# Performance work log

Hardware: AMD Instinct MI355X
Metric: run time of the kernel (lower is better)

## Reference

```python
import jax, jax.numpy as jnp
import numpy as np

VOCAB = 50257
EMBED = 1024


def setup_inputs() -> dict:
    key = jax.random.key(0)
    ks = jax.random.split(key, 8)
    s = 1.0 / np.sqrt(EMBED)  # PyTorch LSTM init scale (for realistic magnitudes)
    return {
        "input": jax.random.randint(ks[0], (1,), 0, VOCAB, dtype=jnp.int64),
        "hidden_state": jax.random.normal(ks[1], (1, 1, EMBED), dtype=jnp.float32),
        "cell_state": jax.random.normal(ks[2], (1, 1, EMBED), dtype=jnp.float32),
        "embed_table": jax.random.normal(ks[3], (VOCAB, EMBED), dtype=jnp.float32),
        "W_ih": jax.random.normal(ks[4], (4 * EMBED, EMBED), dtype=jnp.float32) * s,
        "W_hh": jax.random.normal(ks[5], (4 * EMBED, EMBED), dtype=jnp.float32) * s,
        "b_ih": jax.random.normal(ks[6], (4 * EMBED,), dtype=jnp.float32) * s,
        "b_hh": jax.random.normal(ks[7], (4 * EMBED,), dtype=jnp.float32) * s,
    }


def reference(input, hidden_state, cell_state, embed_table, W_ih, W_hh, b_ih, b_hh):
    # Embedding lookup: token id -> [EMBED]
    x = embed_table[input[0]]                      # [E]
    h = hidden_state[0, 0]                         # [E]
    c = cell_state[0, 0]                           # [E]
    # Single LSTM step, PyTorch gate order: i, f, g, o
    gates = W_ih @ x + b_ih + W_hh @ h + b_hh      # [4E]
    i, f, g, o = jnp.split(gates, 4)
    i = jax.nn.sigmoid(i)
    f = jax.nn.sigmoid(f)
    g = jnp.tanh(g)
    o = jax.nn.sigmoid(o)
    c_new = f * c + i * g
    h_new = o * jnp.tanh(c_new)
    return (h_new.reshape(1, 1, EMBED), c_new.reshape(1, 1, EMBED))
```

## Files before the change

### kernel.cpp

```cpp
#include <hip/hip_runtime.h>
#include <math.h>

#define EMBED 1024

__device__ __forceinline__ float dot4(float4 a, float4 b) {
    return a.x * b.x + a.y * b.y + a.z * b.z + a.w * b.w;
}

__global__ __launch_bounds__(256) void lstm_step_kernel(
    const unsigned int* __restrict__ tok,
    const float* __restrict__ h_in,
    const float* __restrict__ c_in,
    const float* __restrict__ embed,
    const float* __restrict__ W_ih,
    const float* __restrict__ W_hh,
    const float* __restrict__ b_ih,
    const float* __restrict__ b_hh,
    float* __restrict__ out)
{
    __shared__ float x_s[EMBED];
    __shared__ float h_s[EMBED];
    __shared__ float gate_s[4];

    const int tid  = threadIdx.x;
    const int j    = blockIdx.x;
    const int w    = tid >> 6;
    const int lane = tid & 63;
    const int row  = w * EMBED + j;

    const float4* wi = (const float4*)(W_ih + (size_t)row * EMBED);
    const float4* wh = (const float4*)(W_hh + (size_t)row * EMBED);
    float4 a0 = wi[lane];
    float4 a1 = wi[lane + 64];
    float4 a2 = wi[lane + 128];
    float4 a3 = wi[lane + 192];
    float4 b0 = wh[lane];
    float4 b1 = wh[lane + 64];
    float4 b2 = wh[lane + 128];
    float4 b3 = wh[lane + 192];

    const float bias  = b_ih[row] + b_hh[row];
    const float c_val = c_in[j];

    const unsigned int t = tok[0];
    const float* xrow = embed + (size_t)t * EMBED;
    ((float4*)x_s)[tid] = ((const float4*)xrow)[tid];
    ((float4*)h_s)[tid] = ((const float4*)h_in)[tid];
    __syncthreads();

    const float4* xs4 = (const float4*)x_s;
    const float4* hs4 = (const float4*)h_s;

    float acc;
    acc  = dot4(a0, xs4[lane]);
    acc += dot4(a1, xs4[lane + 64]);
    acc += dot4(a2, xs4[lane + 128]);
    acc += dot4(a3, xs4[lane + 192]);
    acc += dot4(b0, hs4[lane]);
    acc += dot4(b1, hs4[lane + 64]);
    acc += dot4(b2, hs4[lane + 128]);
    acc += dot4(b3, hs4[lane + 192]);

    #pragma unroll
    for (int off = 32; off > 0; off >>= 1)
        acc += __shfl_xor(acc, off);

    if (lane == 0)
        gate_s[w] = acc + bias;
    __syncthreads();

    if (tid == 0) {
        const float gi = gate_s[0];
        const float gf = gate_s[1];
        const float gg = gate_s[2];
        const float go = gate_s[3];
        const float i = 1.f / (1.f + __expf(-gi));
        const float f = 1.f / (1.f + __expf(-gf));
        const float e2g = __expf(2.f * gg);
        const float g = (e2g - 1.f) / (e2g + 1.f);
        const float o = 1.f / (1.f + __expf(-go));
        const float c_new = f * c_val + i * g;
        const float e2c = __expf(2.f * c_new);
        const float tc  = (e2c - 1.f) / (e2c + 1.f);
        const float h_new = o * tc;
        out[j]         = h_new;
        out[EMBED + j] = c_new;
    }
}

extern "C" void kernel_launch(void* const* d_in, const int* in_sizes, int n_in,
                              void* d_out, int out_size, void* d_ws, size_t ws_size,
                              hipStream_t stream) {
    const unsigned int* tok  = (const unsigned int*)d_in[0];
    const float* h_in  = (const float*)d_in[1];
    const float* c_in  = (const float*)d_in[2];
    const float* embed = (const float*)d_in[3];
    const float* W_ih  = (const float*)d_in[4];
    const float* W_hh  = (const float*)d_in[5];
    const float* b_ih  = (const float*)d_in[6];
    const float* b_hh  = (const float*)d_in[7];
    float* out = (float*)d_out;

    lstm_step_kernel<<<EMBED, 256, 0, stream>>>(
        tok, h_in, c_in, embed, W_ih, W_hh, b_ih, b_hh, out);
}
```

Before: 9.995 us.

## Split each gate row across two wavefronts and drop shared-memory vector staging

Each block now runs 512 threads (8 wavefronts), giving each of W_ih and W_hh its own wavefront per gate, so each thread loads half as many weight vectors. The x and h vectors are read straight from global memory into registers instead of being staged through LDS, which removes the first __syncthreads. The two partial sums are added in thread 0 before the activations are applied. This raises parallelism and memory-level concurrency on a bandwidth-bound GEMV, at the cost of redundant global reads of x/h that rely on the cache.

```diff
diff --git a/kernel.cpp b/kernel.cpp
--- a/kernel.cpp
+++ b/kernel.cpp
@@ -3,11 +3,13 @@
 
 #define EMBED 1024
 
-__device__ __forceinline__ float dot4(float4 a, float4 b) {
-    return a.x * b.x + a.y * b.y + a.z * b.z + a.w * b.w;
+typedef float f32x4 __attribute__((ext_vector_type(4)));
+
+__device__ __forceinline__ float dot4(f32x4 a, f32x4 b) {
+    return a[0] * b[0] + a[1] * b[1] + a[2] * b[2] + a[3] * b[3];
 }
 
-__global__ __launch_bounds__(256) void lstm_step_kernel(
+__global__ __launch_bounds__(512) void lstm_step_kernel(
     const unsigned int* __restrict__ tok,
     const float* __restrict__ h_in,
     const float* __restrict__ c_in,
@@ -18,62 +20,54 @@
     const float* __restrict__ b_hh,
     float* __restrict__ out)
 {
-    __shared__ float x_s[EMBED];
-    __shared__ float h_s[EMBED];
-    __shared__ float gate_s[4];
+    __shared__ float part[8];
 
     const int tid  = threadIdx.x;
     const int j    = blockIdx.x;
     const int w    = tid >> 6;
     const int lane = tid & 63;
-    const int row  = w * EMBED + j;
+    const int gate = w >> 1;
+    const int half = w & 1;
+    const int row  = gate * EMBED + j;
 
-    const float4* wi = (const float4*)(W_ih + (size_t)row * EMBED);
-    const float4* wh = (const float4*)(W_hh + (size_t)row * EMBED);
-    float4 a0 = wi[lane];
-    float4 a1 = wi[lane + 64];
-    float4 a2 = wi[lane + 128];
-    float4 a3 = wi[lane + 192];
-    float4 b0 = wh[lane];
-    float4 b1 = wh[lane + 64];
-    float4 b2 = wh[lane + 128];
-    float4 b3 = wh[lane + 192];
+    const float* Wm = half ? W_hh : W_ih;
+    const f32x4* wr = (const f32x4*)(Wm + (size_t)row * EMBED);
+    f32x4 a0 = wr[lane];
+    f32x4 a1 = wr[lane + 64];
+    f32x4 a2 = wr[lane + 128];
+    f32x4 a3 = wr[lane + 192];
 
-    const float bias  = b_ih[row] + b_hh[row];
-    const float c_val = c_in[j];
+    const float bias  = half ? b_hh[row] : b_ih[row];
+    const float c_val = (w == 0) ? c_in[j] : 0.f;
 
-    const unsigned int t = tok[0];
-    const float* xrow = embed + (size_t)t * EMBED;
-    ((float4*)x_s)[tid] = ((const float4*)xrow)[tid];
-    ((float4*)h_s)[tid] = ((const float4*)h_in)[tid];
-    __syncthreads();
+    const float* vbase;
+    if (half) {
+        vbase = h_in;
+    } else {
+        const unsigned int t = tok[0];
+        vbase = embed + (size_t)t * EMBED;
+    }
+    const f32x4* v4 = (const f32x4*)vbase;
+    f32x4 b0 = v4[lane];
+    f32x4 b1 = v4[lane + 64];
+    f32x4 b2 = v4[lane + 128];
+    f32x4 b3 = v4[lane + 192];
 
-    const float4* xs4 = (const float4*)x_s;
-    const float4* hs4 = (const float4*)h_s;
-
-    float acc;
-    acc  = dot4(a0, xs4[lane]);
-    acc += dot4(a1, xs4[lane + 64]);
-    acc += dot4(a2, xs4[lane + 128]);
-    acc += dot4(a3, xs4[lane + 192]);
-    acc += dot4(b0, hs4[lane]);
-    acc += dot4(b1, hs4[lane + 64]);
-    acc += dot4(b2, hs4[lane + 128]);
-    acc += dot4(b3, hs4[lane + 192]);
+    float acc = dot4(a0, b0) + dot4(a1, b1) + dot4(a2, b2) + dot4(a3, b3);
 
     #pragma unroll
     for (int off = 32; off > 0; off >>= 1)
         acc += __shfl_xor(acc, off);
 
     if (lane == 0)
-        gate_s[w] = acc + bias;
+        part[w] = acc + bias;
     __syncthreads();
 
     if (tid == 0) {
-        const float gi = gate_s[0];
-        const float gf = gate_s[1];
-        const float gg = gate_s[2];
-        const float go = gate_s[3];
+        const float gi = part[0] + part[1];
+        const float gf = part[2] + part[3];
+        const float gg = part[4] + part[5];
+        const float go = part[6] + part[7];
         const float i = 1.f / (1.f + __expf(-gi));
         const float f = 1.f / (1.f + __expf(-gf));
         const float e2g = __expf(2.f * gg);
@@ -82,8 +76,7 @@
         const float c_new = f * c_val + i * g;
         const float e2c = __expf(2.f * c_new);
         const float tc  = (e2c - 1.f) / (e2c + 1.f);
-        const float h_new = o * tc;
-        out[j]         = h_new;
+        out[j]         = o * tc;
         out[EMBED + j] = c_new;
     }
 }
@@ -101,6 +94,6 @@
     const float* b_hh  = (const float*)d_in[7];
     float* out = (float*)d_out;
 
-    lstm_step_kernel<<<EMBED, 256, 0, stream>>>(
+    lstm_step_kernel<<<EMBED, 512, 0, stream>>>(
         tok, h_in, c_in, embed, W_ih, W_hh, b_ih, b_hh, out);
 }
```

Result: no change. 9.818 us (-1.8%).
